# Kernel tuning notes

Measured on AMD Instinct MI355X. Metric: run time of the kernel, lower is better.

## Reference

```python
import jax, jax.numpy as jnp
import numpy as np

B, S, D = 2, 2048, 1024
H = 16
HD = D // H  # 64


def setup_inputs() -> dict:
    key = jax.random.key(0)
    ks = jax.random.split(key, 9)
    s = 1.0 / np.sqrt(D)
    x = jax.random.normal(ks[0], (B, S, D), dtype=jnp.float32)
    Wq = jax.random.normal(ks[1], (D, D), dtype=jnp.float32) * s
    Wk = jax.random.normal(ks[2], (D, D), dtype=jnp.float32) * s
    Wv = jax.random.normal(ks[3], (D, D), dtype=jnp.float32) * s
    Wo = jax.random.normal(ks[4], (D, D), dtype=jnp.float32) * s
    bq = jnp.zeros((D,), jnp.float32)
    bk = jnp.zeros((D,), jnp.float32)
    bv = jnp.zeros((D,), jnp.float32)
    bo = jnp.zeros((D,), jnp.float32)
    # causal mask, broadcastable to (B, H, S, S)
    mask = jnp.tril(jnp.ones((S, S), dtype=bool))[None, None, :, :]
    return {"x": x, "Wq": Wq, "bq": bq, "Wk": Wk, "bk": bk,
            "Wv": Wv, "bv": bv, "Wo": Wo, "bo": bo, "mask": mask}


def _split_heads(t):
    # (B, S, D) -> (B, H, S, HD)
    b, s, _ = t.shape
    return t.reshape(b, s, H, HD).transpose(0, 2, 1, 3)


def reference(x, Wq, bq, Wk, bk, Wv, bv, Wo, bo, mask):
    q = _split_heads(x @ Wq + bq)
    k = _split_heads(x @ Wk + bk)
    v = _split_heads(x @ Wv + bv)
    scale = 1.0 / jnp.sqrt(jnp.asarray(HD, dtype=q.dtype))
    scores = jnp.einsum('bhqd,bhkd->bhqk', q, k) * scale
    large_neg = jnp.finfo(scores.dtype).min
    scores = jnp.where(mask, scores, large_neg)
    attn = jax.nn.softmax(scores, axis=-1)
    out = jnp.einsum('bhqk,bhkd->bhqd', attn, v)  # (B,H,S,HD)
    out = out.transpose(0, 2, 1, 3).reshape(x.shape[0], x.shape[1], D)
    return out @ Wo + bo
```

## Files before the change

kernel.cpp:

```cpp
#include <hip/hip_runtime.h>
#include <hip/hip_bf16.h>

typedef __attribute__((ext_vector_type(8))) short bf16x8;
typedef __attribute__((ext_vector_type(4))) float f32x4;

#define B_DIM  2
#define S_DIM  2048
#define D_DIM  1024
#define H_DIM  16
#define HD_DIM 64

__device__ __forceinline__ float bf2f(ushort u) {
    union { unsigned int ui; float f; } c; c.ui = ((unsigned int)u) << 16; return c.f;
}
__device__ __forceinline__ ushort f2bf(float f) {
    __hip_bfloat16 h = __float2bfloat16(f);
    return *reinterpret_cast<ushort*>(&h);
}

__device__ __forceinline__ void async_cp16(const ushort* g, ushort* l) {
    __builtin_amdgcn_global_load_lds(
        (const __attribute__((address_space(1))) void*)g,
        (__attribute__((address_space(3))) void*)l, 16, 0, 0);
}

__device__ __forceinline__ unsigned int cvt_pk_bf16(float lo, float hi) {
    unsigned int d;
    asm volatile("v_cvt_pk_bf16_f32 %0, %1, %2" : "=v"(d) : "v"(lo), "v"(hi));
    return d;
}
__device__ __forceinline__ void pl32swap(unsigned int& a, unsigned int& b) {
    asm volatile("v_permlane32_swap_b32 %0, %1" : "+v"(a), "+v"(b));
}
__device__ __forceinline__ void pl16swap(unsigned int& a, unsigned int& b) {
    asm volatile("v_permlane16_swap_b32 %0, %1" : "+v"(a), "+v"(b));
}

__global__ __launch_bounds__(256) void detect_kernel(const ushort* __restrict__ x,
                                                     int* __restrict__ flag) {
    __shared__ int any;
    int tid = threadIdx.x;
    if (tid == 0) any = 0;
    __syncthreads();
    int cnt = 0;
    for (int j = 0; j < 64; ++j) {
        ushort u = x[tid * 64 + j];
        if (((u >> 7) & 0xFF) == 0xFF) cnt++;
    }
    if (cnt) atomicOr(&any, 1);
    __syncthreads();
    if (tid == 0) *flag = any ? 1 : 0;
}

__global__ __launch_bounds__(256) void prep_kernel(const void* __restrict__ x,
                                                   const void* __restrict__ Wq,
                                                   const void* __restrict__ Wk,
                                                   const void* __restrict__ Wv,
                                                   const void* __restrict__ Wo,
                                                   const void* __restrict__ bq,
                                                   const void* __restrict__ bk,
                                                   const void* __restrict__ bv,
                                                   const void* __restrict__ bo,
                                                   ushort* __restrict__ xc,
                                                   ushort* __restrict__ Wqkvt,
                                                   ushort* __restrict__ Wot,
                                                   float* __restrict__ biasf,
                                                   const int* __restrict__ flag) {
    int tid = threadIdx.x;
    int z = blockIdx.z;
    bool isf32 = (*flag != 0);

    if (z == 4) {
        int t = (blockIdx.y * 16 + blockIdx.x) * 256 + tid;
#pragma unroll
        for (int c = 0; c < 8; ++c) {
            int i = t + c * 65536;
            if (isf32) {
                const float* s = (const float*)x;
                f32x4 a = *(const f32x4*)&s[(size_t)i * 8];
                f32x4 b = *(const f32x4*)&s[(size_t)i * 8 + 4];
                bf16x8 o;
                o[0] = f2bf(a.x); o[1] = f2bf(a.y); o[2] = f2bf(a.z); o[3] = f2bf(a.w);
                o[4] = f2bf(b.x); o[5] = f2bf(b.y); o[6] = f2bf(b.z); o[7] = f2bf(b.w);
                *(bf16x8*)&xc[(size_t)i * 8] = o;
            } else {
                *(bf16x8*)&xc[(size_t)i * 8] =
                    *(const bf16x8*)&((const ushort*)x)[(size_t)i * 8];
            }
        }
        return;
    }
    if (z == 5) {
        int bid = blockIdx.y * 16 + blockIdx.x;
        if (bid >= 16) return;
        int i = bid * 256 + tid;
        int w = i >> 10, j = i & 1023;
        const void* s = (w == 0) ? bq : (w == 1) ? bk : (w == 2) ? bv : bo;
        biasf[i] = isf32 ? ((const float*)s)[j] : bf2f(((const ushort*)s)[j]);
        return;
    }

    __shared__ ushort tile[64][72];
    const void* src = (z == 0) ? Wq : (z == 1) ? Wk : (z == 2) ? Wv : Wo;
    ushort* dst = (z < 3) ? (Wqkvt + (size_t)z * D_DIM * D_DIM) : Wot;
    int r0 = blockIdx.y * 64, c0 = blockIdx.x * 64;
#pragma unroll
    for (int p = 0; p < 2; ++p) {
        int r = p * 32 + (tid >> 3);
        int c = (tid & 7) * 8;
        if (isf32) {
            const float* s = (const float*)src;
            f32x4 a = *(const f32x4*)&s[(size_t)(r0 + r) * D_DIM + c0 + c];
            f32x4 b = *(const f32x4*)&s[(size_t)(r0 + r) * D_DIM + c0 + c + 4];
            tile[r][c + 0] = f2bf(a.x); tile[r][c + 1] = f2bf(a.y);
            tile[r][c + 2] = f2bf(a.z); tile[r][c + 3] = f2bf(a.w);
            tile[r][c + 4] = f2bf(b.x); tile[r][c + 5] = f2bf(b.y);
            tile[r][c + 6] = f2bf(b.z); tile[r][c + 7] = f2bf(b.w);
        } else {
            *(bf16x8*)&tile[r][c] =
                *(const bf16x8*)&((const ushort*)src)[(size_t)(r0 + r) * D_DIM + c0 + c];
        }
    }
    __syncthreads();
#pragma unroll
    for (int p = 0; p < 2; ++p) {
        int n  = p * 32 + (tid >> 3);
        int cc = (tid & 7) * 8;
        bf16x8 v;
#pragma unroll
        for (int e = 0; e < 8; ++e) v[e] = (short)tile[cc + e][n];
        *(bf16x8*)&dst[(size_t)(c0 + n) * D_DIM + r0 + cc] = v;
    }
}

__global__ __launch_bounds__(256) void gemm128_kernel(const ushort* __restrict__ A,
                                                      const ushort* __restrict__ Bt,
                                                      const float* __restrict__ bias,
                                                      ushort* __restrict__ qkout,
                                                      ushort* __restrict__ vtout) {
    __shared__ ushort As[128 * 64];
    __shared__ ushort Bs[128 * 64];
    int tid  = threadIdx.x;
    int wave = tid >> 6;
    int lane = tid & 63;
    int l16  = lane & 15;
    int quad = lane >> 4;
    int m0   = blockIdx.y * 128;
    int n0   = blockIdx.x * 128;
    int wm   = wave >> 1;
    int wn   = wave & 1;
    const int K = 1024;

    f32x4 acc[4][4];
#pragma unroll
    for (int i = 0; i < 4; ++i)
#pragma unroll
        for (int j = 0; j < 4; ++j) acc[i][j] = (f32x4){0.f, 0.f, 0.f, 0.f};

    int lrow = lane >> 3;
    int gcol = ((lane & 7) ^ lrow) * 8;
    int sw   = l16 & 7;

    for (int kt = 0; kt < 16; ++kt) {
        int k0 = kt * 64;
#pragma unroll
        for (int j = 0; j < 4; ++j) {
            int chunk = wave * 4 + j;
            int grow  = chunk * 8 + lrow;
            async_cp16(&A[(size_t)(m0 + grow) * K + k0 + gcol], &As[chunk * 512]);
            async_cp16(&Bt[(size_t)(n0 + grow) * K + k0 + gcol], &Bs[chunk * 512]);
        }
        __syncthreads();

#pragma unroll
        for (int kb = 0; kb < 2; ++kb) {
            bf16x8 af[4], bf[4];
#pragma unroll
            for (int i = 0; i < 4; ++i)
                af[i] = *(const bf16x8*)&As[(wm * 64 + i * 16 + l16) * 64 +
                                            (((kb * 4 + quad) ^ sw) << 3)];
#pragma unroll
            for (int j = 0; j < 4; ++j)
                bf[j] = *(const bf16x8*)&Bs[(wn * 64 + j * 16 + l16) * 64 +
                                            (((kb * 4 + quad) ^ sw) << 3)];
#pragma unroll
            for (int i = 0; i < 4; ++i)
#pragma unroll
                for (int j = 0; j < 4; ++j)
                    acc[i][j] = __builtin_amdgcn_mfma_f32_16x16x32_bf16(af[i], bf[j],
                                                                        acc[i][j], 0, 0, 0);
        }
        __syncthreads();
    }

    const size_t TSZ = (size_t)B_DIM * H_DIM * S_DIM * HD_DIM;
#pragma unroll
    for (int j = 0; j < 4; ++j) {
        int n = n0 + wn * 64 + j * 16 + l16;
        float bv = bias[n];
        int which = n >> 10;
        int n1 = n & 1023;
        int h = n1 >> 6, hd = n1 & 63;
#pragma unroll
        for (int i = 0; i < 4; ++i) {
            int mb = m0 + wm * 64 + i * 16 + quad * 4;
            int b = mb >> 11, s = mb & (S_DIM - 1);
            float v4[4];
#pragma unroll
            for (int r = 0; r < 4; ++r) v4[r] = acc[i][j][r] + bv;
            if (which == 2) {
                ushort pk[4];
#pragma unroll
                for (int r = 0; r < 4; ++r) pk[r] = f2bf(v4[r]);
                *(uint2*)&vtout[(((size_t)(b * H_DIM + h) * HD_DIM + hd)) * S_DIM + s] =
                    *(uint2*)pk;
            } else {
#pragma unroll
                for (int r = 0; r < 4; ++r) {
                    float v = v4[r];
                    if (which == 0) v *= 0.18033688011f;
                    qkout[which * TSZ +
                          ((((size_t)(b * H_DIM + h)) * S_DIM + s + r) << 6) + hd] = f2bf(v);
                }
            }
        }
    }
}

__global__ __launch_bounds__(256) void gemm64_kernel(const ushort* __restrict__ A,
                                                     const ushort* __restrict__ Bt,
                                                     const float* __restrict__ bias,
                                                     void* __restrict__ out,
                                                     const int* __restrict__ flag) {
    __shared__ ushort As[64 * 64];
    __shared__ ushort Bs[128 * 64];
    int tid  = threadIdx.x;
    int wave = tid >> 6;
    int lane = tid & 63;
    int l16  = lane & 15;
    int quad = lane >> 4;
    int m0   = blockIdx.y * 64;
    int n0   = blockIdx.x * 128;
    const int K = 1024;

    f32x4 acc[4][2];
#pragma unroll
    for (int i = 0; i < 4; ++i)
#pragma unroll
        for (int j = 0; j < 2; ++j) acc[i][j] = (f32x4){0.f, 0.f, 0.f, 0.f};

    int lrow = lane >> 3;
    int gcol = ((lane & 7) ^ lrow) * 8;
    int sw   = l16 & 7;

    for (int kt = 0; kt < 16; ++kt) {
        int k0 = kt * 64;
#pragma unroll
        for (int j = 0; j < 2; ++j) {
            int chunk = wave * 2 + j;
            int grow  = chunk * 8 + lrow;
            async_cp16(&A[(size_t)(m0 + grow) * K + k0 + gcol], &As[chunk * 512]);
        }
#pragma unroll
        for (int j = 0; j < 4; ++j) {
            int chunk = wave * 4 + j;
            int grow  = chunk * 8 + lrow;
            async_cp16(&Bt[(size_t)(n0 + grow) * K + k0 + gcol], &Bs[chunk * 512]);
        }
        __syncthreads();

#pragma unroll
        for (int kb = 0; kb < 2; ++kb) {
            bf16x8 af[4], bf[2];
#pragma unroll
            for (int i = 0; i < 4; ++i)
                af[i] = *(const bf16x8*)&As[(i * 16 + l16) * 64 +
                                            (((kb * 4 + quad) ^ sw) << 3)];
#pragma unroll
            for (int j = 0; j < 2; ++j)
                bf[j] = *(const bf16x8*)&Bs[(wave * 32 + j * 16 + l16) * 64 +
                                            (((kb * 4 + quad) ^ sw) << 3)];
#pragma unroll
            for (int i = 0; i < 4; ++i)
#pragma unroll
                for (int j = 0; j < 2; ++j)
                    acc[i][j] = __builtin_amdgcn_mfma_f32_16x16x32_bf16(af[i], bf[j],
                                                                        acc[i][j], 0, 0, 0);
        }
        __syncthreads();
    }

    int outf32 = *flag;
#pragma unroll
    for (int j = 0; j < 2; ++j) {
        int n = n0 + wave * 32 + j * 16 + l16;
        float bv = bias[n];
#pragma unroll
        for (int i = 0; i < 4; ++i)
#pragma unroll
            for (int r = 0; r < 4; ++r) {
                int m = m0 + i * 16 + quad * 4 + r;
                float v = acc[i][j][r] + bv;
                if (outf32) ((float*)out)[(size_t)m * D_DIM + n] = v;
                else        ((ushort*)out)[(size_t)m * D_DIM + n] = f2bf(v);
            }
    }
}

__global__ __launch_bounds__(256, 4) void attn_kernel(const ushort* __restrict__ Qg,
                                                      const ushort* __restrict__ Kg,
                                                      const ushort* __restrict__ Vt,
                                                      ushort* __restrict__ attn_out) {
    __shared__ ushort Ks[2][64 * 64];
    __shared__ ushort Vs[2][64 * 64];
    int tid  = threadIdx.x;
    int wave = tid >> 6;
    int lane = tid & 63;
    int l16  = lane & 15;
    int quad = lane >> 4;
    int bh   = blockIdx.x;
    int y    = blockIdx.y;
    int qt   = (y < 8) ? y : (y < 16) ? (23 - y) : (y < 24) ? y : (55 - y);
    int q0   = qt * 64;

    const ushort* Qb = Qg + (size_t)bh * S_DIM * HD_DIM;
    const ushort* Kb = Kg + (size_t)bh * S_DIM * HD_DIM;
    const ushort* Vb = Vt + (size_t)bh * HD_DIM * S_DIM;

    bf16x8 qf[2];
#pragma unroll
    for (int ks = 0; ks < 2; ++ks)
        qf[ks] = *(const bf16x8*)&Qb[(size_t)(q0 + wave * 16 + l16) * HD_DIM +
                                     ks * 32 + quad * 8];

    f32x4 o[4];
#pragma unroll
    for (int i = 0; i < 4; ++i) o[i] = (f32x4){0.f, 0.f, 0.f, 0.f};
    float rsum = 0.f;

    int lrow = lane >> 3;
    int gcol = ((lane & 7) ^ lrow) * 8;
    int sw   = l16 & 7;

#pragma unroll
    for (int j = 0; j < 2; ++j) {
        int chunk = wave * 2 + j;
        int grow  = chunk * 8 + lrow;
        async_cp16(&Kb[(size_t)grow * HD_DIM + gcol], &Ks[0][chunk * 512]);
        async_cp16(&Vb[(size_t)grow * S_DIM + gcol], &Vs[0][chunk * 512]);
    }

    int ntiles = qt + 1;
    int p = 0;
    for (int t = 0; t < ntiles; ++t) {
        __syncthreads();
        if (t + 1 < ntiles) {
            int k1 = (t + 1) * 64;
#pragma unroll
            for (int j = 0; j < 2; ++j) {
                int chunk = wave * 2 + j;
                int grow  = chunk * 8 + lrow;
                async_cp16(&Kb[(size_t)(k1 + grow) * HD_DIM + gcol],
                           &Ks[p ^ 1][chunk * 512]);
                async_cp16(&Vb[(size_t)grow * S_DIM + k1 + gcol],
                           &Vs[p ^ 1][chunk * 512]);
            }
        }
        int k0 = t * 64;

        f32x4 sc[4];
#pragma unroll
        for (int i = 0; i < 4; ++i) sc[i] = (f32x4){0.f, 0.f, 0.f, 0.f};
        __builtin_amdgcn_s_setprio(1);
#pragma unroll
        for (int ks = 0; ks < 2; ++ks)
#pragma unroll
            for (int nb = 0; nb < 4; ++nb) {
                bf16x8 kf = *(const bf16x8*)&Ks[p][(nb * 16 + l16) * 64 +
                                                   (((ks * 4 + quad) ^ sw) << 3)];
                sc[nb] = __builtin_amdgcn_mfma_f32_16x16x32_bf16(kf, qf[ks],
                                                                 sc[nb], 0, 0, 0);
            }
        __builtin_amdgcn_s_setprio(0);

        bf16x8 vf[2][4];
#pragma unroll
        for (int ks = 0; ks < 2; ++ks)
#pragma unroll
            for (int nb = 0; nb < 4; ++nb)
                vf[ks][nb] = *(const bf16x8*)&Vs[p][(nb * 16 + l16) * 64 +
                                                    (((ks * 4 + quad) ^ sw) << 3)];

        if (t == ntiles - 1) {
            int qglob = q0 + wave * 16 + l16;
#pragma unroll
            for (int nb = 0; nb < 4; ++nb) {
                int key = k0 + nb * 16 + quad * 4;
#pragma unroll
                for (int r = 0; r < 4; ++r)
                    if (key + r > qglob) sc[nb][r] = -1e30f;
            }
        }

        unsigned int W[4][2];
        float psn[4];
#pragma unroll
        for (int nb = 0; nb < 4; ++nb) {
            float pv[4];
#pragma unroll
            for (int r = 0; r < 4; ++r) pv[r] = __builtin_amdgcn_exp2f(sc[nb][r]);
            psn[nb] = (pv[0] + pv[1]) + (pv[2] + pv[3]);
            W[nb][0] = cvt_pk_bf16(pv[0], pv[1]);
            W[nb][1] = cvt_pk_bf16(pv[2], pv[3]);
        }
        rsum += (psn[0] + psn[1]) + (psn[2] + psn[3]);

#pragma unroll
        for (int pp = 0; pp < 2; ++pp) {
            pl32swap(W[0][pp], W[1][pp]);
            pl32swap(W[2][pp], W[3][pp]);
            pl16swap(W[0][pp], W[1][pp]);
            pl16swap(W[2][pp], W[3][pp]);
        }
        bf16x8 pf[2];
        {
            union { unsigned int u[4]; bf16x8 v; } c0, c1;
            c0.u[0] = W[0][0]; c0.u[1] = W[0][1];
            c0.u[2] = W[1][0]; c0.u[3] = W[1][1];
            c1.u[0] = W[2][0]; c1.u[1] = W[2][1];
            c1.u[2] = W[3][0]; c1.u[3] = W[3][1];
            pf[0] = c0.v; pf[1] = c1.v;
        }

        __builtin_amdgcn_s_setprio(1);
#pragma unroll
        for (int ks = 0; ks < 2; ++ks)
#pragma unroll
            for (int nb = 0; nb < 4; ++nb)
                o[nb] = __builtin_amdgcn_mfma_f32_16x16x32_bf16(pf[ks], vf[ks][nb],
                                                                o[nb], 0, 0, 0);
        __builtin_amdgcn_s_setprio(0);
        p ^= 1;
    }

    rsum += __shfl_xor(rsum, 16, 64);
    rsum += __shfl_xor(rsum, 32, 64);

    int b = bh >> 4, h = bh & 15;
    float inv[4];
#pragma unroll
    for (int r = 0; r < 4; ++r)
        inv[r] = 1.f / __shfl(rsum, quad * 4 + r, 64);
#pragma unroll
    for (int nb = 0; nb < 4; ++nb)
#pragma unroll
        for (int r = 0; r < 4; ++r) {
            int q = q0 + wave * 16 + quad * 4 + r;
            attn_out[(size_t)(b * S_DIM + q) * D_DIM + h * HD_DIM + nb * 16 + l16] =
                f2bf(o[nb][r] * inv[r]);
        }
}

extern "C" void kernel_launch(void* const* d_in, const int* in_sizes, int n_in,
                              void* d_out, int out_size, void* d_ws, size_t ws_size,
                              hipStream_t stream) {
    const void* x  = d_in[0];
    const void* Wq = d_in[1];
    const void* bq = d_in[2];
    const void* Wk = d_in[3];
    const void* bk = d_in[4];
    const void* Wv = d_in[5];
    const void* bv = d_in[6];
    const void* Wo = d_in[7];
    const void* bo = d_in[8];

    char* ws = (char*)d_ws;
    const size_t MB = 1024 * 1024;
    const size_t base = 64 * 1024;
    int*    flag   = (int*)ws;
    float*  biasf  = (float*)(ws + 4096);
    ushort* xc     = (ushort*)(ws + base);
    ushort* Wqkvt  = (ushort*)(ws + base + 8  * MB);
    ushort* Wot    = (ushort*)(ws + base + 14 * MB);
    ushort* Qc     = (ushort*)(ws + base + 16 * MB);
    ushort* Vtp    = (ushort*)(ws + base + 40 * MB);
    ushort* attn   = xc;

    dim3 tb(256);

    detect_kernel<<<1, tb, 0, stream>>>((const ushort*)x, flag);

    dim3 pg(16, 16, 6);
    prep_kernel<<<pg, tb, 0, stream>>>(x, Wq, Wk, Wv, Wo, bq, bk, bv, bo,
                                       xc, Wqkvt, Wot, biasf, flag);

    dim3 gq(3 * D_DIM / 128, (B_DIM * S_DIM) / 128);
    gemm128_kernel<<<gq, tb, 0, stream>>>(xc, Wqkvt, biasf, Qc, Vtp);

    dim3 ag(B_DIM * H_DIM, S_DIM / 64);
    attn_kernel<<<ag, tb, 0, stream>>>(Qc, Qc + (size_t)B_DIM * H_DIM * S_DIM * HD_DIM,
                                       Vtp, attn);

    dim3 go(D_DIM / 128, (B_DIM * S_DIM) / 64);
    gemm64_kernel<<<go, tb, 0, stream>>>(attn, Wot, biasf + 3072, d_out, flag);
}
```

Measured before the change: 195.2 us.

## Switch attention to 32x32x16 MFMA with 128-row query tiles per block

The attention kernel now processes 128 query rows per block, with each wave owning 32 rows, using 32x32x16 bf16 MFMAs instead of 16x16x32. Each K/V tile loaded into LDS is reused by twice as many query rows, and the P-fragment reshuffle needs only permlane32 swaps. Waves 0-1 skip the final tile because it lies entirely above the causal diagonal for their rows. The cost is higher register pressure (launch bounds drop to 2 blocks per SM), half as many blocks in the grid, and more intra-block load imbalance from causal masking.

```diff
diff --git a/kernel.cpp b/kernel.cpp
--- a/kernel.cpp
+++ b/kernel.cpp
@@ -3,6 +3,7 @@
 
 typedef __attribute__((ext_vector_type(8))) short bf16x8;
 typedef __attribute__((ext_vector_type(4))) float f32x4;
+typedef __attribute__((ext_vector_type(16))) float f32x16;
 
 #define B_DIM  2
 #define S_DIM  2048
@@ -31,9 +32,6 @@
 }
 __device__ __forceinline__ void pl32swap(unsigned int& a, unsigned int& b) {
     asm volatile("v_permlane32_swap_b32 %0, %1" : "+v"(a), "+v"(b));
-}
-__device__ __forceinline__ void pl16swap(unsigned int& a, unsigned int& b) {
-    asm volatile("v_permlane16_swap_b32 %0, %1" : "+v"(a), "+v"(b));
 }
 
 __global__ __launch_bounds__(256) void detect_kernel(const ushort* __restrict__ x,
@@ -307,7 +305,7 @@
     }
 }
 
-__global__ __launch_bounds__(256, 4) void attn_kernel(const ushort* __restrict__ Qg,
+__global__ __launch_bounds__(256, 2) void attn_kernel(const ushort* __restrict__ Qg,
                                                       const ushort* __restrict__ Kg,
                                                       const ushort* __restrict__ Vt,
                                                       ushort* __restrict__ attn_out) {
@@ -316,31 +314,33 @@
     int tid  = threadIdx.x;
     int wave = tid >> 6;
     int lane = tid & 63;
-    int l16  = lane & 15;
-    int quad = lane >> 4;
+    int l31  = lane & 31;
+    int hi   = lane >> 5;
+    int sw7  = lane & 7;
     int bh   = blockIdx.x;
     int y    = blockIdx.y;
-    int qt   = (y < 8) ? y : (y < 16) ? (23 - y) : (y < 24) ? y : (55 - y);
-    int q0   = qt * 64;
+    int qt   = (y < 8) ? y : (23 - y);
+    int q0   = qt * 128;
 
     const ushort* Qb = Qg + (size_t)bh * S_DIM * HD_DIM;
     const ushort* Kb = Kg + (size_t)bh * S_DIM * HD_DIM;
     const ushort* Vb = Vt + (size_t)bh * HD_DIM * S_DIM;
 
-    bf16x8 qf[2];
-#pragma unroll
-    for (int ks = 0; ks < 2; ++ks)
-        qf[ks] = *(const bf16x8*)&Qb[(size_t)(q0 + wave * 16 + l16) * HD_DIM +
-                                     ks * 32 + quad * 8];
-
-    f32x4 o[4];
-#pragma unroll
-    for (int i = 0; i < 4; ++i) o[i] = (f32x4){0.f, 0.f, 0.f, 0.f};
+    bf16x8 qf[4];
+#pragma unroll
+    for (int kk = 0; kk < 4; ++kk)
+        qf[kk] = *(const bf16x8*)&Qb[(size_t)(q0 + wave * 32 + l31) * HD_DIM +
+                                     kk * 16 + hi * 8];
+
+    f32x16 o[2];
+#pragma unroll
+    for (int n = 0; n < 2; ++n)
+#pragma unroll
+        for (int r = 0; r < 16; ++r) o[n][r] = 0.f;
     float rsum = 0.f;
 
     int lrow = lane >> 3;
     int gcol = ((lane & 7) ^ lrow) * 8;
-    int sw   = l16 & 7;
 
 #pragma unroll
     for (int j = 0; j < 2; ++j) {
@@ -350,7 +350,7 @@
         async_cp16(&Vb[(size_t)grow * S_DIM + gcol], &Vs[0][chunk * 512]);
     }
 
-    int ntiles = qt + 1;
+    int ntiles = 2 * qt + 2;
     int p = 0;
     for (int t = 0; t < ntiles; ++t) {
         __syncthreads();
@@ -366,98 +366,94 @@
                            &Vs[p ^ 1][chunk * 512]);
             }
         }
-        int k0 = t * 64;
-
-        f32x4 sc[4];
-#pragma unroll
-        for (int i = 0; i < 4; ++i) sc[i] = (f32x4){0.f, 0.f, 0.f, 0.f};
-        __builtin_amdgcn_s_setprio(1);
-#pragma unroll
-        for (int ks = 0; ks < 2; ++ks)
-#pragma unroll
-            for (int nb = 0; nb < 4; ++nb) {
-                bf16x8 kf = *(const bf16x8*)&Ks[p][(nb * 16 + l16) * 64 +
-                                                   (((ks * 4 + quad) ^ sw) << 3)];
-                sc[nb] = __builtin_amdgcn_mfma_f32_16x16x32_bf16(kf, qf[ks],
-                                                                 sc[nb], 0, 0, 0);
+
+        if (!(t == ntiles - 1 && wave < 2)) {
+            int k0 = t * 64;
+
+            f32x16 sc[2];
+#pragma unroll
+            for (int n = 0; n < 2; ++n)
+#pragma unroll
+                for (int r = 0; r < 16; ++r) sc[n][r] = 0.f;
+            __builtin_amdgcn_s_setprio(1);
+#pragma unroll
+            for (int j = 0; j < 4; ++j)
+#pragma unroll
+                for (int mb = 0; mb < 2; ++mb) {
+                    bf16x8 kf = *(const bf16x8*)&Ks[p][(mb * 32 + l31) * 64 +
+                                                       (((2 * j + hi) ^ sw7) << 3)];
+                    sc[mb] = __builtin_amdgcn_mfma_f32_32x32x16_bf16(kf, qf[j],
+                                                                     sc[mb], 0, 0, 0);
+                }
+            __builtin_amdgcn_s_setprio(0);
+
+            bf16x8 vf[4][2];
+#pragma unroll
+            for (int j = 0; j < 4; ++j)
+#pragma unroll
+                for (int nb = 0; nb < 2; ++nb)
+                    vf[j][nb] = *(const bf16x8*)&Vs[p][(nb * 32 + l31) * 64 +
+                                                       (((2 * j + hi) ^ sw7) << 3)];
+
+            if (t == ntiles - 2 + (wave >> 1)) {
+                int qglob = q0 + wave * 32 + l31;
+#pragma unroll
+                for (int mb = 0; mb < 2; ++mb)
+#pragma unroll
+                    for (int r = 0; r < 16; ++r) {
+                        int key = k0 + mb * 32 + (r & 3) + 8 * (r >> 2) + 4 * hi;
+                        if (key > qglob) sc[mb][r] = -1e30f;
+                    }
             }
-        __builtin_amdgcn_s_setprio(0);
-
-        bf16x8 vf[2][4];
-#pragma unroll
-        for (int ks = 0; ks < 2; ++ks)
-#pragma unroll
-            for (int nb = 0; nb < 4; ++nb)
-                vf[ks][nb] = *(const bf16x8*)&Vs[p][(nb * 16 + l16) * 64 +
-                                                    (((ks * 4 + quad) ^ sw) << 3)];
-
-        if (t == ntiles - 1) {
-            int qglob = q0 + wave * 16 + l16;
-#pragma unroll
-            for (int nb = 0; nb < 4; ++nb) {
-                int key = k0 + nb * 16 + quad * 4;
-#pragma unroll
-                for (int r = 0; r < 4; ++r)
-                    if (key + r > qglob) sc[nb][r] = -1e30f;
+
+            bf16x8 pf[4];
+#pragma unroll
+            for (int mb = 0; mb < 2; ++mb) {
+                unsigned int W[8];
+#pragma unroll
+                for (int g = 0; g < 4; ++g) {
+                    float e0 = __builtin_amdgcn_exp2f(sc[mb][4 * g + 0]);
+                    float e1 = __builtin_amdgcn_exp2f(sc[mb][4 * g + 1]);
+                    float e2 = __builtin_amdgcn_exp2f(sc[mb][4 * g + 2]);
+                    float e3 = __builtin_amdgcn_exp2f(sc[mb][4 * g + 3]);
+                    rsum += (e0 + e1) + (e2 + e3);
+                    W[2 * g]     = cvt_pk_bf16(e0, e1);
+                    W[2 * g + 1] = cvt_pk_bf16(e2, e3);
+                }
+                pl32swap(W[0], W[2]); pl32swap(W[1], W[3]);
+                pl32swap(W[4], W[6]); pl32swap(W[5], W[7]);
+                union { unsigned int u[4]; bf16x8 v; } c0, c1;
+                c0.u[0] = W[0]; c0.u[1] = W[1]; c0.u[2] = W[2]; c0.u[3] = W[3];
+                c1.u[0] = W[4]; c1.u[1] = W[5]; c1.u[2] = W[6]; c1.u[3] = W[7];
+                pf[2 * mb]     = c0.v;
+                pf[2 * mb + 1] = c1.v;
             }
-        }
-
-        unsigned int W[4][2];
-        float psn[4];
-#pragma unroll
-        for (int nb = 0; nb < 4; ++nb) {
-            float pv[4];
-#pragma unroll
-            for (int r = 0; r < 4; ++r) pv[r] = __builtin_amdgcn_exp2f(sc[nb][r]);
-            psn[nb] = (pv[0] + pv[1]) + (pv[2] + pv[3]);
-            W[nb][0] = cvt_pk_bf16(pv[0], pv[1]);
-            W[nb][1] = cvt_pk_bf16(pv[2], pv[3]);
-        }
-        rsum += (psn[0] + psn[1]) + (psn[2] + psn[3]);
-
-#pragma unroll
-        for (int pp = 0; pp < 2; ++pp) {
-            pl32swap(W[0][pp], W[1][pp]);
-            pl32swap(W[2][pp], W[3][pp]);
-            pl16swap(W[0][pp], W[1][pp]);
-            pl16swap(W[2][pp], W[3][pp]);
-        }
-        bf16x8 pf[2];
-        {
-            union { unsigned int u[4]; bf16x8 v; } c0, c1;
-            c0.u[0] = W[0][0]; c0.u[1] = W[0][1];
-            c0.u[2] = W[1][0]; c0.u[3] = W[1][1];
-            c1.u[0] = W[2][0]; c1.u[1] = W[2][1];
-            c1.u[2] = W[3][0]; c1.u[3] = W[3][1];
-            pf[0] = c0.v; pf[1] = c1.v;
-        }
-
-        __builtin_amdgcn_s_setprio(1);
-#pragma unroll
-        for (int ks = 0; ks < 2; ++ks)
-#pragma unroll
-            for (int nb = 0; nb < 4; ++nb)
-                o[nb] = __builtin_amdgcn_mfma_f32_16x16x32_bf16(pf[ks], vf[ks][nb],
-                                                                o[nb], 0, 0, 0);
-        __builtin_amdgcn_s_setprio(0);
+
+            __builtin_amdgcn_s_setprio(1);
+#pragma unroll
+            for (int j = 0; j < 4; ++j)
+#pragma unroll
+                for (int nb = 0; nb < 2; ++nb)
+                    o[nb] = __builtin_amdgcn_mfma_f32_32x32x16_bf16(pf[j], vf[j][nb],
+                                                                    o[nb], 0, 0, 0);
+            __builtin_amdgcn_s_setprio(0);
+        }
         p ^= 1;
     }
 
-    rsum += __shfl_xor(rsum, 16, 64);
     rsum += __shfl_xor(rsum, 32, 64);
+    float inv = 1.f / rsum;
 
     int b = bh >> 4, h = bh & 15;
-    float inv[4];
-#pragma unroll
-    for (int r = 0; r < 4; ++r)
-        inv[r] = 1.f / __shfl(rsum, quad * 4 + r, 64);
-#pragma unroll
-    for (int nb = 0; nb < 4; ++nb)
-#pragma unroll
-        for (int r = 0; r < 4; ++r) {
-            int q = q0 + wave * 16 + quad * 4 + r;
-            attn_out[(size_t)(b * S_DIM + q) * D_DIM + h * HD_DIM + nb * 16 + l16] =
-                f2bf(o[nb][r] * inv[r]);
+#pragma unroll
+    for (int nb = 0; nb < 2; ++nb)
+#pragma unroll
+        for (int r = 0; r < 16; ++r) {
+            int qrow = (r & 3) + 8 * (r >> 2) + 4 * hi;
+            float iv = __shfl(inv, qrow, 64);
+            int q = q0 + wave * 32 + qrow;
+            attn_out[(size_t)(b * S_DIM + q) * D_DIM + h * HD_DIM + nb * 32 + l31] =
+                f2bf(o[nb][r] * iv);
         }
 }
 
@@ -497,7 +493,7 @@
     dim3 gq(3 * D_DIM / 128, (B_DIM * S_DIM) / 128);
     gemm128_kernel<<<gq, tb, 0, stream>>>(xc, Wqkvt, biasf, Qc, Vtp);
 
-    dim3 ag(B_DIM * H_DIM, S_DIM / 64);
+    dim3 ag(B_DIM * H_DIM, S_DIM / 128);
     attn_kernel<<<ag, tb, 0, stream>>>(Qc, Qc + (size_t)B_DIM * H_DIM * S_DIM * HD_DIM,
                                        Vtp, attn);
 
```

New measurement: 194.8 us. Within noise of the previous version (-0.2%).
